# Performance work log

Hardware: AMD Instinct MI355X
Metric: run time of the kernel (lower is better)

## Reference

```python
import jax, jax.numpy as jnp
import numpy as np

S, B, E = 128, 64, 512          # seqlen, batch, incoming feature dim
P_LEN, P_DIM = 160, 512         # post length, post_size
H = 1024                        # hidden_size; GRU input_size = E + P_DIM = 1024
NEG = -1000000000.0             # masked_fill value in maskedSoftmax


def setup_inputs() -> dict:
    key = jax.random.key(0)
    ks = jax.random.split(key, 11)
    s = 1.0 / np.sqrt(H)
    u = lambda k, shp: jax.random.uniform(k, shp, jnp.float32, -s, s)
    return {
        "incoming": jax.random.normal(ks[0], (S, B, E), jnp.float32),
        "post": jax.random.normal(ks[1], (P_LEN, B, P_DIM), jnp.float32),
        "h_init": u(ks[2], (1, 1, H)),
        "weight_ih": u(ks[3], (3 * H, E + P_DIM)),
        "weight_hh": u(ks[4], (3 * H, H)),
        "bias_ih": u(ks[5], (3 * H,)),
        "bias_hh": u(ks[6], (3 * H,)),
        "wq": u(ks[7], (P_DIM, H)),
        "bq": u(ks[8], (P_DIM,)),
        "length": jax.random.randint(ks[9], (B,), 1, S + 1),
        "post_length": jax.random.randint(ks[10], (B,), 1, P_LEN + 1),
    }


def reference(incoming, post, h_init, weight_ih, weight_hh, bias_ih, bias_hh,
              wq, bq, length, post_length):
    seqlen, batch = incoming.shape[0], incoming.shape[1]
    plen = post.shape[0]
    h0 = jnp.broadcast_to(h_init[0], (batch, h_init.shape[-1]))  # h_init.repeat(1,B,1)[0]
    pos_mask = jnp.arange(plen)[:, None] < post_length[None, :]  # [P, B]

    def step(h, xt_i):
        xt, i = xt_i
        # attention over post, softmax along post-length axis (dim 0)
        query = h @ wq.T + bq                                   # [B, P_DIM]
        scores = jnp.einsum('pbd,bd->pb', post, query)          # [P, B]
        attn = jax.nn.softmax(jnp.where(pos_mask, scores, NEG), axis=0)
        context = jnp.einsum('pb,pbd->bd', attn, post)          # [B, P_DIM]
        x = jnp.concatenate([xt, context], axis=-1)             # [B, E + P_DIM]
        # torch GRUCell (gate order: r, z, n)
        gi = x @ weight_ih.T + bias_ih                          # [B, 3H]
        gh = h @ weight_hh.T + bias_hh                          # [B, 3H]
        i_r, i_z, i_n = jnp.split(gi, 3, axis=-1)
        h_r, h_z, h_n = jnp.split(gh, 3, axis=-1)
        r = jax.nn.sigmoid(i_r + h_r)
        z = jax.nn.sigmoid(i_z + h_z)
        n = jnp.tanh(i_n + r * h_n)
        h_new = (1.0 - z) * n + z * h
        # zero out finished sequences: h_now * (length > i)
        h_new = h_new * (length > i)[:, None].astype(h.dtype)
        return h_new, h_new

    h_last, hs = jax.lax.scan(step, h0, (incoming, jnp.arange(seqlen)))
    return hs, h_last
```

## Files before the change

### kernel.cpp

```cpp
#include <hip/hip_runtime.h>

#define S_LEN 128
#define BATCH 64
#define EDIM  512
#define PLEN  160
#define PDIM  512
#define HDIM  1024
#define G3    3072
#define NBLK  128
#define NTHR  256
#define PROWS 144

typedef _Float16 half8v  __attribute__((ext_vector_type(8)));
typedef _Float16 half4v  __attribute__((ext_vector_type(4)));
typedef _Float16 half2v  __attribute__((ext_vector_type(2)));
typedef float    f32x4   __attribute__((ext_vector_type(4)));

#define CTRL_UINTS 24576
#define OFF_CTRL ((size_t)0)
#define OFF_WIH  ((size_t)(CTRL_UINTS*4))
#define OFF_WHH  (OFF_WIH  + (size_t)G3*HDIM*2)
#define OFF_WQH  (OFF_WHH  + (size_t)G3*HDIM*2)
#define OFF_INC  (OFF_WQH  + (size_t)PDIM*HDIM*2)
#define OFF_POST (OFF_INC  + (size_t)S_LEN*BATCH*EDIM*2)
#define OFF_HH   (OFF_POST + (size_t)PLEN*BATCH*PDIM*2)
#define OFF_QH   (OFF_HH   + (size_t)BATCH*HDIM*2)
#define OFF_CTX  (OFF_QH   + (size_t)BATCH*PDIM*2)

__global__ void init_ctrl(unsigned* u) {
    int i = threadIdx.x + blockIdx.x * blockDim.x;
    if (i < CTRL_UINTS) u[i] = 0u;
}

__device__ __forceinline__ float wave_sum(float v) {
    v += __shfl_xor(v, 32); v += __shfl_xor(v, 16); v += __shfl_xor(v, 8);
    v += __shfl_xor(v, 4);  v += __shfl_xor(v, 2);  v += __shfl_xor(v, 1);
    return v;
}
__device__ __forceinline__ float wave_max(float v) {
    v = fmaxf(v, __shfl_xor(v, 32)); v = fmaxf(v, __shfl_xor(v, 16));
    v = fmaxf(v, __shfl_xor(v, 8));  v = fmaxf(v, __shfl_xor(v, 4));
    v = fmaxf(v, __shfl_xor(v, 2));  v = fmaxf(v, __shfl_xor(v, 1));
    return v;
}

__device__ __forceinline__ void gbar(unsigned* arrive, unsigned& gen, int tid, int blk) {
    gen++;
    __syncthreads();
    if (tid == 0)
        __hip_atomic_store(&arrive[blk * 32], gen, __ATOMIC_RELEASE, __HIP_MEMORY_SCOPE_AGENT);
    if (tid < NBLK) {
        unsigned* fl = &arrive[tid * 32];
        while (__hip_atomic_load(fl, __ATOMIC_RELAXED, __HIP_MEMORY_SCOPE_AGENT) < gen) { }
        __hip_atomic_load(fl, __ATOMIC_ACQUIRE, __HIP_MEMORY_SCOPE_AGENT);
    }
    __syncthreads();
}

__device__ __forceinline__ void mfma_acc(f32x4& acc, const _Float16* __restrict__ A, int lda,
                                         const _Float16* __restrict__ Bb, int ldb,
                                         int ksteps, int lane) {
    const _Float16* ap = A  + (size_t)(lane & 15) * lda + ((lane >> 4) << 3);
    const _Float16* bp = Bb + (size_t)(lane & 15) * ldb + ((lane >> 4) << 3);
    #pragma unroll
    for (int ks = 0; ks < ksteps; ++ks) {
        half8v av = *(const half8v*)ap;
        half8v bv = *(const half8v*)bp;
        acc = __builtin_amdgcn_mfma_f32_16x16x32_f16(av, bv, acc, 0, 0, 0);
        ap += 32; bp += 32;
    }
}

__device__ __forceinline__ void mfma_acc3(f32x4& a0, f32x4& a1, f32x4& a2,
        const _Float16* __restrict__ A, int lda,
        const _Float16* __restrict__ B0, const _Float16* __restrict__ B1,
        const _Float16* __restrict__ B2, int ldb, int ksteps, int lane) {
    const _Float16* ap = A  + (size_t)(lane & 15) * lda + ((lane >> 4) << 3);
    const _Float16* p0 = B0 + (size_t)(lane & 15) * ldb + ((lane >> 4) << 3);
    const _Float16* p1 = B1 + (size_t)(lane & 15) * ldb + ((lane >> 4) << 3);
    const _Float16* p2 = B2 + (size_t)(lane & 15) * ldb + ((lane >> 4) << 3);
    #pragma unroll
    for (int ks = 0; ks < ksteps; ++ks) {
        half8v av = *(const half8v*)ap;
        a0 = __builtin_amdgcn_mfma_f32_16x16x32_f16(av, *(const half8v*)p0, a0, 0, 0, 0);
        a1 = __builtin_amdgcn_mfma_f32_16x16x32_f16(av, *(const half8v*)p1, a1, 0, 0, 0);
        a2 = __builtin_amdgcn_mfma_f32_16x16x32_f16(av, *(const half8v*)p2, a2, 0, 0, 0);
        ap += 32; p0 += 32; p1 += 32; p2 += 32;
    }
}

__global__ __launch_bounds__(NTHR, 1) void gru_main(
    const float* __restrict__ incoming, const float* __restrict__ post,
    const float* __restrict__ h_init,   const float* __restrict__ w_ih,
    const float* __restrict__ w_hh,     const float* __restrict__ b_ih,
    const float* __restrict__ b_hh,     const float* __restrict__ wq,
    const float* __restrict__ bq,       const int* __restrict__ length,
    const int* __restrict__ post_length, float* __restrict__ out,
    char* __restrict__ ws)
{
    const int tid  = threadIdx.x;
    const int blk  = blockIdx.x;
    const int lane = tid & 63;
    const int wv   = tid >> 6;

    unsigned* arrive = (unsigned*)(ws + OFF_CTRL);
    unsigned* qflag  = (unsigned*)(ws + OFF_CTRL) + 4096;
    _Float16* wih_h  = (_Float16*)(ws + OFF_WIH);
    _Float16* whh_h  = (_Float16*)(ws + OFF_WHH);
    _Float16* wq_h   = (_Float16*)(ws + OFF_WQH);
    _Float16* inc_h  = (_Float16*)(ws + OFF_INC);
    _Float16* post_h = (_Float16*)(ws + OFF_POST);
    _Float16* h_h    = (_Float16*)(ws + OFF_HH);
    _Float16* query_h= (_Float16*)(ws + OFF_QH);
    _Float16* ctx_h  = (_Float16*)(ws + OFF_CTX);

    __shared__ __align__(16) _Float16 s_post[PROWS * PDIM];
    __shared__ __align__(16) _Float16 s_q[PDIM];
    __shared__ float s_scores[PLEN];
    __shared__ float s_w[PLEN];
    __shared__ float s_bc[2];

    unsigned gen = 0;

    float bsr = 0.f, bsz = 0.f, bin_ = 0.f, bhn = 0.f, bqv = 0.f;
    float hp[4] = {0.f, 0.f, 0.f, 0.f};
    int lenb[4] = {0, 0, 0, 0};
    int j0 = 0, ab = 0, plen = 0;
    if (blk < 64) {
        j0 = blk * 16;
        const int j = j0 + (lane & 15);
        bsr  = b_ih[j] + b_hh[j];
        bsz  = b_ih[HDIM + j] + b_hh[HDIM + j];
        bin_ = b_ih[2*HDIM + j];
        bhn  = b_hh[2*HDIM + j];
        if (blk < 32) bqv = bq[blk*16 + (lane & 15)];
        const float hi = h_init[j];
        const int r0 = wv*16 + ((lane >> 4) << 2);
        #pragma unroll
        for (int r = 0; r < 4; ++r) { hp[r] = hi; lenb[r] = length[r0 + r]; }
    } else {
        ab = blk - 64;
        plen = post_length[ab];
    }

    {
        const int NV4_W    = G3*HDIM/4;
        const int NV4_WQ   = PDIM*HDIM/4;
        const int NV4_INC  = S_LEN*BATCH*EDIM/4;
        const int NV4_POST = PLEN*BATCH*PDIM/4;
        const int TOT = 2*NV4_W + NV4_WQ + NV4_INC + NV4_POST;
        for (int i = blk*NTHR + tid; i < TOT; i += NBLK*NTHR) {
            const float* s; _Float16* dp; int o;
            if (i < NV4_W)                          { s = w_ih;     dp = wih_h;  o = i; }
            else if (i < 2*NV4_W)                   { s = w_hh;     dp = whh_h;  o = i - NV4_W; }
            else if (i < 2*NV4_W + NV4_WQ)          { s = wq;       dp = wq_h;   o = i - 2*NV4_W; }
            else if (i < 2*NV4_W + NV4_WQ + NV4_INC){ s = incoming; dp = inc_h;  o = i - 2*NV4_W - NV4_WQ; }
            else                                    { s = post;     dp = post_h; o = i - 2*NV4_W - NV4_WQ - NV4_INC; }
            f32x4 v = *(const f32x4*)(s + (size_t)o*4);
            half4v hv4 = {(_Float16)v.x, (_Float16)v.y, (_Float16)v.z, (_Float16)v.w};
            *(half4v*)(dp + (size_t)o*4) = hv4;
        }
        for (int i = blk*NTHR + tid; i < BATCH*HDIM; i += NBLK*NTHR)
            h_h[i] = (_Float16)h_init[i & (HDIM-1)];
    }
    if (blk >= 64) {
        for (int i = tid; i < PROWS*PDIM; i += NTHR) {
            const int p = i >> 9, d = i & (PDIM-1);
            s_post[i] = (_Float16)post[((size_t)p*BATCH + ab)*PDIM + d];
        }
    }
    gbar(arrive, gen, tid, blk);

    for (int t = 0; t < S_LEN; ++t) {
        f32x4 ghr = {0.f,0.f,0.f,0.f}, ghz = {0.f,0.f,0.f,0.f}, ghn_ = {0.f,0.f,0.f,0.f};
        f32x4 gir = {0.f,0.f,0.f,0.f}, giz = {0.f,0.f,0.f,0.f}, gin_ = {0.f,0.f,0.f,0.f};

        if (blk < 64) {
            if (blk < 32) {
                const int q0 = blk * 16;
                f32x4 qa = {0.f,0.f,0.f,0.f};
                mfma_acc(qa, h_h + (size_t)(wv*16)*HDIM, HDIM,
                         wq_h + (size_t)q0*HDIM, HDIM, HDIM/32, lane);
                const int q  = q0 + (lane & 15);
                const int r0 = wv*16 + ((lane >> 4) << 2);
                #pragma unroll
                for (int r = 0; r < 4; ++r)
                    query_h[(size_t)(r0+r)*PDIM + q] = (_Float16)(qa[r] + bqv);
                __syncthreads();
                if (tid == 0)
                    __hip_atomic_store(&qflag[blk * 32], (unsigned)(t+1),
                                       __ATOMIC_RELEASE, __HIP_MEMORY_SCOPE_AGENT);
            }
            mfma_acc3(ghr, ghz, ghn_, h_h + (size_t)(wv*16)*HDIM, HDIM,
                      whh_h + (size_t)j0*HDIM,
                      whh_h + (size_t)(HDIM + j0)*HDIM,
                      whh_h + (size_t)(2*HDIM + j0)*HDIM, HDIM, HDIM/32, lane);
            mfma_acc3(gir, giz, gin_, inc_h + ((size_t)t*BATCH + wv*16)*EDIM, EDIM,
                      wih_h + (size_t)j0*HDIM,
                      wih_h + (size_t)(HDIM + j0)*HDIM,
                      wih_h + (size_t)(2*HDIM + j0)*HDIM, HDIM, EDIM/32, lane);
        } else {
            half8v srow[4];
            #pragma unroll
            for (int i = 0; i < 4; ++i)
                srow[i] = *(const half8v*)(post_h +
                            ((size_t)(PROWS + wv + 4*i)*BATCH + ab)*PDIM + lane*8);
            if (tid < 32) {
                unsigned* fl = &qflag[tid * 32];
                while (__hip_atomic_load(fl, __ATOMIC_RELAXED, __HIP_MEMORY_SCOPE_AGENT) < (unsigned)(t+1)) { }
                __hip_atomic_load(fl, __ATOMIC_ACQUIRE, __HIP_MEMORY_SCOPE_AGENT);
            }
            __syncthreads();
            if (tid < PDIM/8)
                *(half8v*)&s_q[tid*8] = *(const half8v*)&query_h[(size_t)ab*PDIM + tid*8];
            __syncthreads();
            const half8v qv = *(const half8v*)&s_q[lane*8];
            #pragma unroll 2
            for (int p = wv; p < PROWS; p += 4) {
                const half8v pv = *(const half8v*)&s_post[(size_t)p*PDIM + lane*8];
                float sd = 0.f;
                #pragma unroll
                for (int jj = 0; jj < 8; ++jj) sd += (float)pv[jj] * (float)qv[jj];
                sd = wave_sum(sd);
                if (lane == 0) s_scores[p] = sd;
            }
            #pragma unroll
            for (int i = 0; i < 4; ++i) {
                const half8v pv = srow[i];
                float sd = 0.f;
                #pragma unroll
                for (int jj = 0; jj < 8; ++jj) sd += (float)pv[jj] * (float)qv[jj];
                sd = wave_sum(sd);
                if (lane == 0) s_scores[PROWS + wv + 4*i] = sd;
            }
            __syncthreads();
            if (wv == 0) {
                float m = -1e30f;
                for (int p = lane; p < plen; p += 64) m = fmaxf(m, s_scores[p]);
                m = wave_max(m);
                if (lane == 0) s_bc[0] = m;
            }
            __syncthreads();
            const float mx = s_bc[0];
            if (tid < PLEN) s_w[tid] = (tid < plen) ? __expf(s_scores[tid] - mx) : 0.f;
            __syncthreads();
            if (wv == 0) {
                float ss = 0.f;
                for (int p = lane; p < PLEN; p += 64) ss += s_w[p];
                ss = wave_sum(ss);
                if (lane == 0) s_bc[1] = 1.f / ss;
            }
            __syncthreads();
            const float inv_den = s_bc[1];
            const int d0 = tid << 1;
            float ca = 0.f, cb = 0.f;
            #pragma unroll 4
            for (int p = 0; p < PROWS; ++p) {
                const half2v pv2 = *(const half2v*)&s_post[(size_t)p*PDIM + d0];
                const float wp = s_w[p];
                ca += wp * (float)pv2[0];
                cb += wp * (float)pv2[1];
            }
            #pragma unroll 4
            for (int p = PROWS; p < PLEN; ++p) {
                const half2v pv2 = *(const half2v*)(post_h + ((size_t)p*BATCH + ab)*PDIM + d0);
                const float wp = s_w[p];
                ca += wp * (float)pv2[0];
                cb += wp * (float)pv2[1];
            }
            half2v cv; cv[0] = (_Float16)(ca * inv_den); cv[1] = (_Float16)(cb * inv_den);
            *(half2v*)&ctx_h[(size_t)ab*PDIM + d0] = cv;
        }
        gbar(arrive, gen, tid, blk);

        if (blk < 64) {
            mfma_acc3(gir, giz, gin_, ctx_h + (size_t)(wv*16)*PDIM, PDIM,
                      wih_h + (size_t)j0*HDIM + PDIM,
                      wih_h + (size_t)(HDIM + j0)*HDIM + PDIM,
                      wih_h + (size_t)(2*HDIM + j0)*HDIM + PDIM, HDIM, PDIM/32, lane);
            const int j  = j0 + (lane & 15);
            const int r0 = wv*16 + ((lane >> 4) << 2);
            #pragma unroll
            for (int r = 0; r < 4; ++r) {
                const int b = r0 + r;
                const float rg = 1.f / (1.f + __expf(-(gir[r] + ghr[r] + bsr)));
                const float zg = 1.f / (1.f + __expf(-(giz[r] + ghz[r] + bsz)));
                const float e2 = __expf(2.f * ((gin_[r] + bin_) + rg * (ghn_[r] + bhn)));
                const float ng = 1.f - 2.f / (e2 + 1.f);
                float hv = (1.f - zg) * ng + zg * hp[r];
                if (lenb[r] <= t) hv = 0.f;
                hp[r] = hv;
                out[(size_t)t*BATCH*HDIM + (size_t)b*HDIM + j] = hv;
                h_h[(size_t)b*HDIM + j] = (_Float16)hv;
                if (t == S_LEN - 1)
                    out[(size_t)S_LEN*BATCH*HDIM + (size_t)b*HDIM + j] = hv;
            }
        }
        if (t < S_LEN - 1) gbar(arrive, gen, tid, blk);
    }
}

extern "C" void kernel_launch(void* const* d_in, const int* in_sizes, int n_in,
                              void* d_out, int out_size, void* d_ws, size_t ws_size,
                              hipStream_t stream) {
    (void)in_sizes; (void)n_in; (void)out_size; (void)ws_size;
    const float* incoming    = (const float*)d_in[0];
    const float* post        = (const float*)d_in[1];
    const float* h_init      = (const float*)d_in[2];
    const float* w_ih        = (const float*)d_in[3];
    const float* w_hh        = (const float*)d_in[4];
    const float* b_ih        = (const float*)d_in[5];
    const float* b_hh        = (const float*)d_in[6];
    const float* wq          = (const float*)d_in[7];
    const float* bq          = (const float*)d_in[8];
    const int*   length      = (const int*)d_in[9];
    const int*   post_length = (const int*)d_in[10];
    float* out = (float*)d_out;

    init_ctrl<<<96, 256, 0, stream>>>((unsigned*)d_ws);
    gru_main<<<NBLK, NTHR, 0, stream>>>(incoming, post, h_init, w_ih, w_hh, b_ih, b_hh,
                                        wq, bq, length, post_length, out, (char*)d_ws);
}
```

Baseline: 5.778 ms.

## Replace persistent grid-barrier kernel with per-timestep kernel launches

The single persistent kernel, which used software grid barriers and flag spinning, is split into a staging kernel plus three kernels per timestep (query, attention, gate) launched 128 times. Kernel boundaries now provide the synchronisation, and a double-buffered fp16 hidden state replaces in-place updates. The cost is 384 extra launches, and the attention kernel reloads its post slice into shared memory on every step instead of keeping it resident. The query GEMM is also spread over 128 single-wave blocks instead of sharing blocks with the gate work.

```diff
diff --git a/kernel.cpp b/kernel.cpp
--- a/kernel.cpp
+++ b/kernel.cpp
@@ -7,8 +7,6 @@
 #define PDIM  512
 #define HDIM  1024
 #define G3    3072
-#define NBLK  128
-#define NTHR  256
 #define PROWS 144
 
 typedef _Float16 half8v  __attribute__((ext_vector_type(8)));
@@ -16,21 +14,14 @@
 typedef _Float16 half2v  __attribute__((ext_vector_type(2)));
 typedef float    f32x4   __attribute__((ext_vector_type(4)));
 
-#define CTRL_UINTS 24576
-#define OFF_CTRL ((size_t)0)
-#define OFF_WIH  ((size_t)(CTRL_UINTS*4))
+#define OFF_WIH  ((size_t)0)
 #define OFF_WHH  (OFF_WIH  + (size_t)G3*HDIM*2)
 #define OFF_WQH  (OFF_WHH  + (size_t)G3*HDIM*2)
 #define OFF_INC  (OFF_WQH  + (size_t)PDIM*HDIM*2)
 #define OFF_POST (OFF_INC  + (size_t)S_LEN*BATCH*EDIM*2)
-#define OFF_HH   (OFF_POST + (size_t)PLEN*BATCH*PDIM*2)
-#define OFF_QH   (OFF_HH   + (size_t)BATCH*HDIM*2)
+#define OFF_HB   (OFF_POST + (size_t)PLEN*BATCH*PDIM*2)
+#define OFF_QH   (OFF_HB   + (size_t)2*BATCH*HDIM*2)
 #define OFF_CTX  (OFF_QH   + (size_t)BATCH*PDIM*2)
-
-__global__ void init_ctrl(unsigned* u) {
-    int i = threadIdx.x + blockIdx.x * blockDim.x;
-    if (i < CTRL_UINTS) u[i] = 0u;
-}
 
 __device__ __forceinline__ float wave_sum(float v) {
     v += __shfl_xor(v, 32); v += __shfl_xor(v, 16); v += __shfl_xor(v, 8);
@@ -42,19 +33,6 @@
     v = fmaxf(v, __shfl_xor(v, 8));  v = fmaxf(v, __shfl_xor(v, 4));
     v = fmaxf(v, __shfl_xor(v, 2));  v = fmaxf(v, __shfl_xor(v, 1));
     return v;
-}
-
-__device__ __forceinline__ void gbar(unsigned* arrive, unsigned& gen, int tid, int blk) {
-    gen++;
-    __syncthreads();
-    if (tid == 0)
-        __hip_atomic_store(&arrive[blk * 32], gen, __ATOMIC_RELEASE, __HIP_MEMORY_SCOPE_AGENT);
-    if (tid < NBLK) {
-        unsigned* fl = &arrive[tid * 32];
-        while (__hip_atomic_load(fl, __ATOMIC_RELAXED, __HIP_MEMORY_SCOPE_AGENT) < gen) { }
-        __hip_atomic_load(fl, __ATOMIC_ACQUIRE, __HIP_MEMORY_SCOPE_AGENT);
-    }
-    __syncthreads();
 }
 
 __device__ __forceinline__ void mfma_acc(f32x4& acc, const _Float16* __restrict__ A, int lda,
@@ -89,30 +67,69 @@
     }
 }
 
-__global__ __launch_bounds__(NTHR, 1) void gru_main(
-    const float* __restrict__ incoming, const float* __restrict__ post,
-    const float* __restrict__ h_init,   const float* __restrict__ w_ih,
-    const float* __restrict__ w_hh,     const float* __restrict__ b_ih,
-    const float* __restrict__ b_hh,     const float* __restrict__ wq,
-    const float* __restrict__ bq,       const int* __restrict__ length,
-    const int* __restrict__ post_length, float* __restrict__ out,
+__global__ __launch_bounds__(256) void k_stage(
+    const float* __restrict__ w_ih, const float* __restrict__ w_hh,
+    const float* __restrict__ wq,   const float* __restrict__ incoming,
+    const float* __restrict__ post, const float* __restrict__ h_init,
     char* __restrict__ ws)
 {
-    const int tid  = threadIdx.x;
-    const int blk  = blockIdx.x;
-    const int lane = tid & 63;
-    const int wv   = tid >> 6;
-
-    unsigned* arrive = (unsigned*)(ws + OFF_CTRL);
-    unsigned* qflag  = (unsigned*)(ws + OFF_CTRL) + 4096;
     _Float16* wih_h  = (_Float16*)(ws + OFF_WIH);
     _Float16* whh_h  = (_Float16*)(ws + OFF_WHH);
     _Float16* wq_h   = (_Float16*)(ws + OFF_WQH);
     _Float16* inc_h  = (_Float16*)(ws + OFF_INC);
     _Float16* post_h = (_Float16*)(ws + OFF_POST);
-    _Float16* h_h    = (_Float16*)(ws + OFF_HH);
-    _Float16* query_h= (_Float16*)(ws + OFF_QH);
-    _Float16* ctx_h  = (_Float16*)(ws + OFF_CTX);
+    _Float16* hb     = (_Float16*)(ws + OFF_HB);
+    const int NV4_W    = G3*HDIM/4;
+    const int NV4_WQ   = PDIM*HDIM/4;
+    const int NV4_INC  = S_LEN*BATCH*EDIM/4;
+    const int NV4_POST = PLEN*BATCH*PDIM/4;
+    const int TOT = 2*NV4_W + NV4_WQ + NV4_INC + NV4_POST;
+    const int gs = gridDim.x * blockDim.x;
+    for (int i = blockIdx.x*blockDim.x + threadIdx.x; i < TOT; i += gs) {
+        const float* s; _Float16* dp; int o;
+        if (i < NV4_W)                          { s = w_ih;     dp = wih_h;  o = i; }
+        else if (i < 2*NV4_W)                   { s = w_hh;     dp = whh_h;  o = i - NV4_W; }
+        else if (i < 2*NV4_W + NV4_WQ)          { s = wq;       dp = wq_h;   o = i - 2*NV4_W; }
+        else if (i < 2*NV4_W + NV4_WQ + NV4_INC){ s = incoming; dp = inc_h;  o = i - 2*NV4_W - NV4_WQ; }
+        else                                    { s = post;     dp = post_h; o = i - 2*NV4_W - NV4_WQ - NV4_INC; }
+        f32x4 v = *(const f32x4*)(s + (size_t)o*4);
+        half4v hv4 = {(_Float16)v.x, (_Float16)v.y, (_Float16)v.z, (_Float16)v.w};
+        *(half4v*)(dp + (size_t)o*4) = hv4;
+    }
+    for (int i = blockIdx.x*blockDim.x + threadIdx.x; i < BATCH*HDIM; i += gs)
+        hb[i] = (_Float16)h_init[i & (HDIM-1)];
+}
+
+__global__ __launch_bounds__(64) void k_query(
+    const float* __restrict__ bq, int t, char* __restrict__ ws)
+{
+    const int lane = threadIdx.x;
+    const int mt = blockIdx.x >> 5;
+    const int nt = blockIdx.x & 31;
+    const _Float16* hb   = (const _Float16*)(ws + OFF_HB) + (size_t)(t & 1)*BATCH*HDIM;
+    const _Float16* wq_h = (const _Float16*)(ws + OFF_WQH);
+    _Float16* query_h    = (_Float16*)(ws + OFF_QH);
+    f32x4 qa = {0.f,0.f,0.f,0.f};
+    mfma_acc(qa, hb + (size_t)(mt*16)*HDIM, HDIM,
+             wq_h + (size_t)(nt*16)*HDIM, HDIM, HDIM/32, lane);
+    const int col = nt*16 + (lane & 15);
+    const int r0  = mt*16 + ((lane >> 4) << 2);
+    const float b = bq[col];
+    #pragma unroll
+    for (int r = 0; r < 4; ++r)
+        query_h[(size_t)(r0+r)*PDIM + col] = (_Float16)(qa[r] + b);
+}
+
+__global__ __launch_bounds__(256) void k_attn(
+    const int* __restrict__ post_length, int t, char* __restrict__ ws)
+{
+    const int tid  = threadIdx.x;
+    const int lane = tid & 63;
+    const int wv   = tid >> 6;
+    const int ab   = blockIdx.x;
+    const _Float16* post_h  = (const _Float16*)(ws + OFF_POST);
+    const _Float16* query_h = (const _Float16*)(ws + OFF_QH);
+    _Float16* ctx_h         = (_Float16*)(ws + OFF_CTX);
 
     __shared__ __align__(16) _Float16 s_post[PROWS * PDIM];
     __shared__ __align__(16) _Float16 s_q[PDIM];
@@ -120,183 +137,131 @@
     __shared__ float s_w[PLEN];
     __shared__ float s_bc[2];
 
-    unsigned gen = 0;
-
-    float bsr = 0.f, bsz = 0.f, bin_ = 0.f, bhn = 0.f, bqv = 0.f;
-    float hp[4] = {0.f, 0.f, 0.f, 0.f};
-    int lenb[4] = {0, 0, 0, 0};
-    int j0 = 0, ab = 0, plen = 0;
-    if (blk < 64) {
-        j0 = blk * 16;
-        const int j = j0 + (lane & 15);
-        bsr  = b_ih[j] + b_hh[j];
-        bsz  = b_ih[HDIM + j] + b_hh[HDIM + j];
-        bin_ = b_ih[2*HDIM + j];
-        bhn  = b_hh[2*HDIM + j];
-        if (blk < 32) bqv = bq[blk*16 + (lane & 15)];
-        const float hi = h_init[j];
-        const int r0 = wv*16 + ((lane >> 4) << 2);
+    const int plen = post_length[ab];
+    for (int i = tid; i < PROWS*PDIM/8; i += 256) {
+        const int p = i >> 6, v = i & 63;
+        ((half8v*)s_post)[i] = *(const half8v*)(post_h + ((size_t)p*BATCH + ab)*PDIM + v*8);
+    }
+    half8v srow[4];
+    #pragma unroll
+    for (int i = 0; i < 4; ++i)
+        srow[i] = *(const half8v*)(post_h + ((size_t)(PROWS + wv + 4*i)*BATCH + ab)*PDIM + lane*8);
+    if (tid < PDIM/8)
+        *(half8v*)&s_q[tid*8] = *(const half8v*)&query_h[(size_t)ab*PDIM + tid*8];
+    __syncthreads();
+
+    const half8v qv = *(const half8v*)&s_q[lane*8];
+    #pragma unroll 2
+    for (int p = wv; p < PROWS; p += 4) {
+        const half8v pv = *(const half8v*)&s_post[(size_t)p*PDIM + lane*8];
+        float sd = 0.f;
         #pragma unroll
-        for (int r = 0; r < 4; ++r) { hp[r] = hi; lenb[r] = length[r0 + r]; }
-    } else {
-        ab = blk - 64;
-        plen = post_length[ab];
-    }
-
-    {
-        const int NV4_W    = G3*HDIM/4;
-        const int NV4_WQ   = PDIM*HDIM/4;
-        const int NV4_INC  = S_LEN*BATCH*EDIM/4;
-        const int NV4_POST = PLEN*BATCH*PDIM/4;
-        const int TOT = 2*NV4_W + NV4_WQ + NV4_INC + NV4_POST;
-        for (int i = blk*NTHR + tid; i < TOT; i += NBLK*NTHR) {
-            const float* s; _Float16* dp; int o;
-            if (i < NV4_W)                          { s = w_ih;     dp = wih_h;  o = i; }
-            else if (i < 2*NV4_W)                   { s = w_hh;     dp = whh_h;  o = i - NV4_W; }
-            else if (i < 2*NV4_W + NV4_WQ)          { s = wq;       dp = wq_h;   o = i - 2*NV4_W; }
-            else if (i < 2*NV4_W + NV4_WQ + NV4_INC){ s = incoming; dp = inc_h;  o = i - 2*NV4_W - NV4_WQ; }
-            else                                    { s = post;     dp = post_h; o = i - 2*NV4_W - NV4_WQ - NV4_INC; }
-            f32x4 v = *(const f32x4*)(s + (size_t)o*4);
-            half4v hv4 = {(_Float16)v.x, (_Float16)v.y, (_Float16)v.z, (_Float16)v.w};
-            *(half4v*)(dp + (size_t)o*4) = hv4;
-        }
-        for (int i = blk*NTHR + tid; i < BATCH*HDIM; i += NBLK*NTHR)
-            h_h[i] = (_Float16)h_init[i & (HDIM-1)];
-    }
-    if (blk >= 64) {
-        for (int i = tid; i < PROWS*PDIM; i += NTHR) {
-            const int p = i >> 9, d = i & (PDIM-1);
-            s_post[i] = (_Float16)post[((size_t)p*BATCH + ab)*PDIM + d];
-        }
-    }
-    gbar(arrive, gen, tid, blk);
-
-    for (int t = 0; t < S_LEN; ++t) {
-        f32x4 ghr = {0.f,0.f,0.f,0.f}, ghz = {0.f,0.f,0.f,0.f}, ghn_ = {0.f,0.f,0.f,0.f};
-        f32x4 gir = {0.f,0.f,0.f,0.f}, giz = {0.f,0.f,0.f,0.f}, gin_ = {0.f,0.f,0.f,0.f};
-
-        if (blk < 64) {
-            if (blk < 32) {
-                const int q0 = blk * 16;
-                f32x4 qa = {0.f,0.f,0.f,0.f};
-                mfma_acc(qa, h_h + (size_t)(wv*16)*HDIM, HDIM,
-                         wq_h + (size_t)q0*HDIM, HDIM, HDIM/32, lane);
-                const int q  = q0 + (lane & 15);
-                const int r0 = wv*16 + ((lane >> 4) << 2);
-                #pragma unroll
-                for (int r = 0; r < 4; ++r)
-                    query_h[(size_t)(r0+r)*PDIM + q] = (_Float16)(qa[r] + bqv);
-                __syncthreads();
-                if (tid == 0)
-                    __hip_atomic_store(&qflag[blk * 32], (unsigned)(t+1),
-                                       __ATOMIC_RELEASE, __HIP_MEMORY_SCOPE_AGENT);
-            }
-            mfma_acc3(ghr, ghz, ghn_, h_h + (size_t)(wv*16)*HDIM, HDIM,
-                      whh_h + (size_t)j0*HDIM,
-                      whh_h + (size_t)(HDIM + j0)*HDIM,
-                      whh_h + (size_t)(2*HDIM + j0)*HDIM, HDIM, HDIM/32, lane);
-            mfma_acc3(gir, giz, gin_, inc_h + ((size_t)t*BATCH + wv*16)*EDIM, EDIM,
-                      wih_h + (size_t)j0*HDIM,
-                      wih_h + (size_t)(HDIM + j0)*HDIM,
-                      wih_h + (size_t)(2*HDIM + j0)*HDIM, HDIM, EDIM/32, lane);
-        } else {
-            half8v srow[4];
-            #pragma unroll
-            for (int i = 0; i < 4; ++i)
-                srow[i] = *(const half8v*)(post_h +
-                            ((size_t)(PROWS + wv + 4*i)*BATCH + ab)*PDIM + lane*8);
-            if (tid < 32) {
-                unsigned* fl = &qflag[tid * 32];
-                while (__hip_atomic_load(fl, __ATOMIC_RELAXED, __HIP_MEMORY_SCOPE_AGENT) < (unsigned)(t+1)) { }
-                __hip_atomic_load(fl, __ATOMIC_ACQUIRE, __HIP_MEMORY_SCOPE_AGENT);
-            }
-            __syncthreads();
-            if (tid < PDIM/8)
-                *(half8v*)&s_q[tid*8] = *(const half8v*)&query_h[(size_t)ab*PDIM + tid*8];
-            __syncthreads();
-            const half8v qv = *(const half8v*)&s_q[lane*8];
-            #pragma unroll 2
-            for (int p = wv; p < PROWS; p += 4) {
-                const half8v pv = *(const half8v*)&s_post[(size_t)p*PDIM + lane*8];
-                float sd = 0.f;
-                #pragma unroll
-                for (int jj = 0; jj < 8; ++jj) sd += (float)pv[jj] * (float)qv[jj];
-                sd = wave_sum(sd);
-                if (lane == 0) s_scores[p] = sd;
-            }
-            #pragma unroll
-            for (int i = 0; i < 4; ++i) {
-                const half8v pv = srow[i];
-                float sd = 0.f;
-                #pragma unroll
-                for (int jj = 0; jj < 8; ++jj) sd += (float)pv[jj] * (float)qv[jj];
-                sd = wave_sum(sd);
-                if (lane == 0) s_scores[PROWS + wv + 4*i] = sd;
-            }
-            __syncthreads();
-            if (wv == 0) {
-                float m = -1e30f;
-                for (int p = lane; p < plen; p += 64) m = fmaxf(m, s_scores[p]);
-                m = wave_max(m);
-                if (lane == 0) s_bc[0] = m;
-            }
-            __syncthreads();
-            const float mx = s_bc[0];
-            if (tid < PLEN) s_w[tid] = (tid < plen) ? __expf(s_scores[tid] - mx) : 0.f;
-            __syncthreads();
-            if (wv == 0) {
-                float ss = 0.f;
-                for (int p = lane; p < PLEN; p += 64) ss += s_w[p];
-                ss = wave_sum(ss);
-                if (lane == 0) s_bc[1] = 1.f / ss;
-            }
-            __syncthreads();
-            const float inv_den = s_bc[1];
-            const int d0 = tid << 1;
-            float ca = 0.f, cb = 0.f;
-            #pragma unroll 4
-            for (int p = 0; p < PROWS; ++p) {
-                const half2v pv2 = *(const half2v*)&s_post[(size_t)p*PDIM + d0];
-                const float wp = s_w[p];
-                ca += wp * (float)pv2[0];
-                cb += wp * (float)pv2[1];
-            }
-            #pragma unroll 4
-            for (int p = PROWS; p < PLEN; ++p) {
-                const half2v pv2 = *(const half2v*)(post_h + ((size_t)p*BATCH + ab)*PDIM + d0);
-                const float wp = s_w[p];
-                ca += wp * (float)pv2[0];
-                cb += wp * (float)pv2[1];
-            }
-            half2v cv; cv[0] = (_Float16)(ca * inv_den); cv[1] = (_Float16)(cb * inv_den);
-            *(half2v*)&ctx_h[(size_t)ab*PDIM + d0] = cv;
-        }
-        gbar(arrive, gen, tid, blk);
-
-        if (blk < 64) {
-            mfma_acc3(gir, giz, gin_, ctx_h + (size_t)(wv*16)*PDIM, PDIM,
-                      wih_h + (size_t)j0*HDIM + PDIM,
-                      wih_h + (size_t)(HDIM + j0)*HDIM + PDIM,
-                      wih_h + (size_t)(2*HDIM + j0)*HDIM + PDIM, HDIM, PDIM/32, lane);
-            const int j  = j0 + (lane & 15);
-            const int r0 = wv*16 + ((lane >> 4) << 2);
-            #pragma unroll
-            for (int r = 0; r < 4; ++r) {
-                const int b = r0 + r;
-                const float rg = 1.f / (1.f + __expf(-(gir[r] + ghr[r] + bsr)));
-                const float zg = 1.f / (1.f + __expf(-(giz[r] + ghz[r] + bsz)));
-                const float e2 = __expf(2.f * ((gin_[r] + bin_) + rg * (ghn_[r] + bhn)));
-                const float ng = 1.f - 2.f / (e2 + 1.f);
-                float hv = (1.f - zg) * ng + zg * hp[r];
-                if (lenb[r] <= t) hv = 0.f;
-                hp[r] = hv;
-                out[(size_t)t*BATCH*HDIM + (size_t)b*HDIM + j] = hv;
-                h_h[(size_t)b*HDIM + j] = (_Float16)hv;
-                if (t == S_LEN - 1)
-                    out[(size_t)S_LEN*BATCH*HDIM + (size_t)b*HDIM + j] = hv;
-            }
-        }
-        if (t < S_LEN - 1) gbar(arrive, gen, tid, blk);
+        for (int jj = 0; jj < 8; ++jj) sd += (float)pv[jj] * (float)qv[jj];
+        sd = wave_sum(sd);
+        if (lane == 0) s_scores[p] = sd;
+    }
+    #pragma unroll
+    for (int i = 0; i < 4; ++i) {
+        const half8v pv = srow[i];
+        float sd = 0.f;
+        #pragma unroll
+        for (int jj = 0; jj < 8; ++jj) sd += (float)pv[jj] * (float)qv[jj];
+        sd = wave_sum(sd);
+        if (lane == 0) s_scores[PROWS + wv + 4*i] = sd;
+    }
+    __syncthreads();
+    if (wv == 0) {
+        float m = -1e30f;
+        for (int p = lane; p < plen; p += 64) m = fmaxf(m, s_scores[p]);
+        m = wave_max(m);
+        if (lane == 0) s_bc[0] = m;
+    }
+    __syncthreads();
+    const float mx = s_bc[0];
+    if (tid < PLEN) s_w[tid] = (tid < plen) ? __expf(s_scores[tid] - mx) : 0.f;
+    __syncthreads();
+    if (wv == 0) {
+        float ss = 0.f;
+        for (int p = lane; p < PLEN; p += 64) ss += s_w[p];
+        ss = wave_sum(ss);
+        if (lane == 0) s_bc[1] = 1.f / ss;
+    }
+    __syncthreads();
+    const float inv_den = s_bc[1];
+    const int d0 = tid << 1;
+    float ca = 0.f, cb = 0.f;
+    #pragma unroll 4
+    for (int p = 0; p < PROWS; ++p) {
+        const half2v pv2 = *(const half2v*)&s_post[(size_t)p*PDIM + d0];
+        const float wp = s_w[p];
+        ca += wp * (float)pv2[0];
+        cb += wp * (float)pv2[1];
+    }
+    #pragma unroll 4
+    for (int p = PROWS; p < PLEN; ++p) {
+        const half2v pv2 = *(const half2v*)(post_h + ((size_t)p*BATCH + ab)*PDIM + d0);
+        const float wp = s_w[p];
+        ca += wp * (float)pv2[0];
+        cb += wp * (float)pv2[1];
+    }
+    half2v cv; cv[0] = (_Float16)(ca * inv_den); cv[1] = (_Float16)(cb * inv_den);
+    *(half2v*)&ctx_h[(size_t)ab*PDIM + d0] = cv;
+}
+
+__global__ __launch_bounds__(256) void k_gate(
+    const float* __restrict__ b_ih, const float* __restrict__ b_hh,
+    const float* __restrict__ h_init, const int* __restrict__ length,
+    float* __restrict__ out, int t, char* __restrict__ ws)
+{
+    const int tid  = threadIdx.x;
+    const int lane = tid & 63;
+    const int wv   = tid >> 6;
+    const int j0   = blockIdx.x * 16;
+    const _Float16* wih_h = (const _Float16*)(ws + OFF_WIH);
+    const _Float16* whh_h = (const _Float16*)(ws + OFF_WHH);
+    const _Float16* inc_h = (const _Float16*)(ws + OFF_INC);
+    const _Float16* ctx_h = (const _Float16*)(ws + OFF_CTX);
+    _Float16* hb          = (_Float16*)(ws + OFF_HB);
+    const _Float16* hin   = hb + (size_t)(t & 1)*BATCH*HDIM;
+    _Float16* hout        = hb + (size_t)((t + 1) & 1)*BATCH*HDIM;
+
+    const int j = j0 + (lane & 15);
+    const float bsr  = b_ih[j] + b_hh[j];
+    const float bsz  = b_ih[HDIM + j] + b_hh[HDIM + j];
+    const float bin_ = b_ih[2*HDIM + j];
+    const float bhn  = b_hh[2*HDIM + j];
+
+    f32x4 ghr = {0.f,0.f,0.f,0.f}, ghz = {0.f,0.f,0.f,0.f}, ghn_ = {0.f,0.f,0.f,0.f};
+    f32x4 gir = {0.f,0.f,0.f,0.f}, giz = {0.f,0.f,0.f,0.f}, gin_ = {0.f,0.f,0.f,0.f};
+    mfma_acc3(ghr, ghz, ghn_, hin + (size_t)(wv*16)*HDIM, HDIM,
+              whh_h + (size_t)j0*HDIM,
+              whh_h + (size_t)(HDIM + j0)*HDIM,
+              whh_h + (size_t)(2*HDIM + j0)*HDIM, HDIM, HDIM/32, lane);
+    mfma_acc3(gir, giz, gin_, inc_h + ((size_t)t*BATCH + wv*16)*EDIM, EDIM,
+              wih_h + (size_t)j0*HDIM,
+              wih_h + (size_t)(HDIM + j0)*HDIM,
+              wih_h + (size_t)(2*HDIM + j0)*HDIM, HDIM, EDIM/32, lane);
+    mfma_acc3(gir, giz, gin_, ctx_h + (size_t)(wv*16)*PDIM, PDIM,
+              wih_h + (size_t)j0*HDIM + PDIM,
+              wih_h + (size_t)(HDIM + j0)*HDIM + PDIM,
+              wih_h + (size_t)(2*HDIM + j0)*HDIM + PDIM, HDIM, PDIM/32, lane);
+
+    const int r0 = wv*16 + ((lane >> 4) << 2);
+    #pragma unroll
+    for (int r = 0; r < 4; ++r) {
+        const int b = r0 + r;
+        const float hp = (t == 0) ? h_init[j] : out[(size_t)(t-1)*BATCH*HDIM + (size_t)b*HDIM + j];
+        const int lenb = length[b];
+        const float rg = 1.f / (1.f + __expf(-(gir[r] + ghr[r] + bsr)));
+        const float zg = 1.f / (1.f + __expf(-(giz[r] + ghz[r] + bsz)));
+        const float e2 = __expf(2.f * ((gin_[r] + bin_) + rg * (ghn_[r] + bhn)));
+        const float ng = 1.f - 2.f / (e2 + 1.f);
+        float hv = (1.f - zg) * ng + zg * hp;
+        if (lenb <= t) hv = 0.f;
+        out[(size_t)t*BATCH*HDIM + (size_t)b*HDIM + j] = hv;
+        hout[(size_t)b*HDIM + j] = (_Float16)hv;
+        if (t == S_LEN - 1)
+            out[(size_t)S_LEN*BATCH*HDIM + (size_t)b*HDIM + j] = hv;
     }
 }
 
@@ -316,8 +281,12 @@
     const int*   length      = (const int*)d_in[9];
     const int*   post_length = (const int*)d_in[10];
     float* out = (float*)d_out;
-
-    init_ctrl<<<96, 256, 0, stream>>>((unsigned*)d_ws);
-    gru_main<<<NBLK, NTHR, 0, stream>>>(incoming, post, h_init, w_ih, w_hh, b_ih, b_hh,
-                                        wq, bq, length, post_length, out, (char*)d_ws);
-}
+    char* ws = (char*)d_ws;
+
+    k_stage<<<256, 256, 0, stream>>>(w_ih, w_hh, wq, incoming, post, h_init, ws);
+    for (int t = 0; t < S_LEN; ++t) {
+        k_query<<<128, 64, 0, stream>>>(bq, t, ws);
+        k_attn<<<64, 256, 0, stream>>>(post_length, t, ws);
+        k_gate<<<64, 256, 0, stream>>>(b_ih, b_hh, h_init, length, out, t, ws);
+    }
+}
```

New measurement: 7.299 ms. 1.26x slower.

## Compute query projection as split-K partials after each GRU update

Applied to the files above, without the earlier changes.

The separate per-step query GEMM (h @ wq^T on 32 blocks, followed by a flag wait) is removed. Each of the 64 GRU blocks now keeps its 16-column slice of wq in shared memory and, right after producing its h slice, writes a partial query product to global memory. The attention blocks then sum the 64 partials themselves, which takes the query computation and its flag synchronization off the critical path at the start of each step. The hidden state is double-buffered so the next step's read does not race with the current write. The cost is extra global traffic: 64×64×512 fp32 partial stores per step and a 64-way reduction in every attention block.

```diff
diff --git a/kernel.cpp b/kernel.cpp
--- a/kernel.cpp
+++ b/kernel.cpp
@@ -20,12 +20,11 @@
 #define OFF_CTRL ((size_t)0)
 #define OFF_WIH  ((size_t)(CTRL_UINTS*4))
 #define OFF_WHH  (OFF_WIH  + (size_t)G3*HDIM*2)
-#define OFF_WQH  (OFF_WHH  + (size_t)G3*HDIM*2)
-#define OFF_INC  (OFF_WQH  + (size_t)PDIM*HDIM*2)
+#define OFF_INC  (OFF_WHH  + (size_t)G3*HDIM*2)
 #define OFF_POST (OFF_INC  + (size_t)S_LEN*BATCH*EDIM*2)
-#define OFF_HH   (OFF_POST + (size_t)PLEN*BATCH*PDIM*2)
-#define OFF_QH   (OFF_HH   + (size_t)BATCH*HDIM*2)
-#define OFF_CTX  (OFF_QH   + (size_t)BATCH*PDIM*2)
+#define OFF_HB   (OFF_POST + (size_t)PLEN*BATCH*PDIM*2)
+#define OFF_CTX  (OFF_HB   + (size_t)2*BATCH*HDIM*2)
+#define OFF_QP   (OFF_CTX  + (size_t)BATCH*PDIM*2)
 
 __global__ void init_ctrl(unsigned* u) {
     int i = threadIdx.x + blockIdx.x * blockDim.x;
@@ -55,20 +54,6 @@
         __hip_atomic_load(fl, __ATOMIC_ACQUIRE, __HIP_MEMORY_SCOPE_AGENT);
     }
     __syncthreads();
-}
-
-__device__ __forceinline__ void mfma_acc(f32x4& acc, const _Float16* __restrict__ A, int lda,
-                                         const _Float16* __restrict__ Bb, int ldb,
-                                         int ksteps, int lane) {
-    const _Float16* ap = A  + (size_t)(lane & 15) * lda + ((lane >> 4) << 3);
-    const _Float16* bp = Bb + (size_t)(lane & 15) * ldb + ((lane >> 4) << 3);
-    #pragma unroll
-    for (int ks = 0; ks < ksteps; ++ks) {
-        half8v av = *(const half8v*)ap;
-        half8v bv = *(const half8v*)bp;
-        acc = __builtin_amdgcn_mfma_f32_16x16x32_f16(av, bv, acc, 0, 0, 0);
-        ap += 32; bp += 32;
-    }
 }
 
 __device__ __forceinline__ void mfma_acc3(f32x4& a0, f32x4& a1, f32x4& a2,
@@ -89,6 +74,24 @@
     }
 }
 
+__device__ __forceinline__ void qpart_mfma(const _Float16* s_hq, const _Float16* s_wqp,
+                                           float* __restrict__ qpart, int blk,
+                                           int lane, int wv) {
+    const int ko = (lane >> 4) << 3;
+    const half8v af = *(const half8v*)(s_hq + (size_t)(wv*16 + (lane & 15))*32 + ko);
+    const int b0 = wv*16 + ((lane >> 4) << 2);
+    #pragma unroll 4
+    for (int nt = 0; nt < 32; ++nt) {
+        const half8v bf = *(const half8v*)(s_wqp + (size_t)(nt*16 + (lane & 15))*32 + ko);
+        f32x4 acc = {0.f,0.f,0.f,0.f};
+        acc = __builtin_amdgcn_mfma_f32_16x16x32_f16(af, bf, acc, 0, 0, 0);
+        const int qc = nt*16 + (lane & 15);
+        #pragma unroll
+        for (int r = 0; r < 4; ++r)
+            qpart[((size_t)blk*BATCH + b0 + r)*PDIM + qc] = acc[r];
+    }
+}
+
 __global__ __launch_bounds__(NTHR, 1) void gru_main(
     const float* __restrict__ incoming, const float* __restrict__ post,
     const float* __restrict__ h_init,   const float* __restrict__ w_ih,
@@ -104,25 +107,25 @@
     const int wv   = tid >> 6;
 
     unsigned* arrive = (unsigned*)(ws + OFF_CTRL);
-    unsigned* qflag  = (unsigned*)(ws + OFF_CTRL) + 4096;
     _Float16* wih_h  = (_Float16*)(ws + OFF_WIH);
     _Float16* whh_h  = (_Float16*)(ws + OFF_WHH);
-    _Float16* wq_h   = (_Float16*)(ws + OFF_WQH);
     _Float16* inc_h  = (_Float16*)(ws + OFF_INC);
     _Float16* post_h = (_Float16*)(ws + OFF_POST);
-    _Float16* h_h    = (_Float16*)(ws + OFF_HH);
-    _Float16* query_h= (_Float16*)(ws + OFF_QH);
+    _Float16* hb     = (_Float16*)(ws + OFF_HB);
     _Float16* ctx_h  = (_Float16*)(ws + OFF_CTX);
+    float*    qpart  = (float*)(ws + OFF_QP);
 
     __shared__ __align__(16) _Float16 s_post[PROWS * PDIM];
     __shared__ __align__(16) _Float16 s_q[PDIM];
     __shared__ float s_scores[PLEN];
     __shared__ float s_w[PLEN];
     __shared__ float s_bc[2];
+    _Float16* s_wqp = s_post;
+    _Float16* s_hq  = s_post + 512*32;
 
     unsigned gen = 0;
 
-    float bsr = 0.f, bsz = 0.f, bin_ = 0.f, bhn = 0.f, bqv = 0.f;
+    float bsr = 0.f, bsz = 0.f, bin_ = 0.f, bhn = 0.f;
     float hp[4] = {0.f, 0.f, 0.f, 0.f};
     int lenb[4] = {0, 0, 0, 0};
     int j0 = 0, ab = 0, plen = 0;
@@ -133,7 +136,6 @@
         bsz  = b_ih[HDIM + j] + b_hh[HDIM + j];
         bin_ = b_ih[2*HDIM + j];
         bhn  = b_hh[2*HDIM + j];
-        if (blk < 32) bqv = bq[blk*16 + (lane & 15)];
         const float hi = h_init[j];
         const int r0 = wv*16 + ((lane >> 4) << 2);
         #pragma unroll
@@ -145,25 +147,34 @@
 
     {
         const int NV4_W    = G3*HDIM/4;
-        const int NV4_WQ   = PDIM*HDIM/4;
         const int NV4_INC  = S_LEN*BATCH*EDIM/4;
         const int NV4_POST = PLEN*BATCH*PDIM/4;
-        const int TOT = 2*NV4_W + NV4_WQ + NV4_INC + NV4_POST;
+        const int TOT = 2*NV4_W + NV4_INC + NV4_POST;
         for (int i = blk*NTHR + tid; i < TOT; i += NBLK*NTHR) {
             const float* s; _Float16* dp; int o;
-            if (i < NV4_W)                          { s = w_ih;     dp = wih_h;  o = i; }
-            else if (i < 2*NV4_W)                   { s = w_hh;     dp = whh_h;  o = i - NV4_W; }
-            else if (i < 2*NV4_W + NV4_WQ)          { s = wq;       dp = wq_h;   o = i - 2*NV4_W; }
-            else if (i < 2*NV4_W + NV4_WQ + NV4_INC){ s = incoming; dp = inc_h;  o = i - 2*NV4_W - NV4_WQ; }
-            else                                    { s = post;     dp = post_h; o = i - 2*NV4_W - NV4_WQ - NV4_INC; }
+            if (i < NV4_W)                  { s = w_ih;     dp = wih_h;  o = i; }
+            else if (i < 2*NV4_W)           { s = w_hh;     dp = whh_h;  o = i - NV4_W; }
+            else if (i < 2*NV4_W + NV4_INC) { s = incoming; dp = inc_h;  o = i - 2*NV4_W; }
+            else                            { s = post;     dp = post_h; o = i - 2*NV4_W - NV4_INC; }
             f32x4 v = *(const f32x4*)(s + (size_t)o*4);
             half4v hv4 = {(_Float16)v.x, (_Float16)v.y, (_Float16)v.z, (_Float16)v.w};
             *(half4v*)(dp + (size_t)o*4) = hv4;
         }
         for (int i = blk*NTHR + tid; i < BATCH*HDIM; i += NBLK*NTHR)
-            h_h[i] = (_Float16)h_init[i & (HDIM-1)];
-    }
-    if (blk >= 64) {
+            hb[i] = (_Float16)h_init[i & (HDIM-1)];
+    }
+    if (blk < 64) {
+        for (int i = tid; i < 512*32; i += NTHR) {
+            const int c = i >> 5, k = i & 31;
+            s_wqp[i] = (k < 16) ? (_Float16)wq[(size_t)c*HDIM + j0 + k] : (_Float16)0.f;
+        }
+        for (int i = tid; i < 64*32; i += NTHR) {
+            const int k = i & 31;
+            s_hq[i] = (k < 16) ? (_Float16)h_init[j0 + k] : (_Float16)0.f;
+        }
+        __syncthreads();
+        qpart_mfma(s_hq, s_wqp, qpart, blk, lane, wv);
+    } else {
         for (int i = tid; i < PROWS*PDIM; i += NTHR) {
             const int p = i >> 9, d = i & (PDIM-1);
             s_post[i] = (_Float16)post[((size_t)p*BATCH + ab)*PDIM + d];
@@ -176,22 +187,7 @@
         f32x4 gir = {0.f,0.f,0.f,0.f}, giz = {0.f,0.f,0.f,0.f}, gin_ = {0.f,0.f,0.f,0.f};
 
         if (blk < 64) {
-            if (blk < 32) {
-                const int q0 = blk * 16;
-                f32x4 qa = {0.f,0.f,0.f,0.f};
-                mfma_acc(qa, h_h + (size_t)(wv*16)*HDIM, HDIM,
-                         wq_h + (size_t)q0*HDIM, HDIM, HDIM/32, lane);
-                const int q  = q0 + (lane & 15);
-                const int r0 = wv*16 + ((lane >> 4) << 2);
-                #pragma unroll
-                for (int r = 0; r < 4; ++r)
-                    query_h[(size_t)(r0+r)*PDIM + q] = (_Float16)(qa[r] + bqv);
-                __syncthreads();
-                if (tid == 0)
-                    __hip_atomic_store(&qflag[blk * 32], (unsigned)(t+1),
-                                       __ATOMIC_RELEASE, __HIP_MEMORY_SCOPE_AGENT);
-            }
-            mfma_acc3(ghr, ghz, ghn_, h_h + (size_t)(wv*16)*HDIM, HDIM,
+            mfma_acc3(ghr, ghz, ghn_, hb + (size_t)(t & 1)*BATCH*HDIM + (size_t)(wv*16)*HDIM, HDIM,
                       whh_h + (size_t)j0*HDIM,
                       whh_h + (size_t)(HDIM + j0)*HDIM,
                       whh_h + (size_t)(2*HDIM + j0)*HDIM, HDIM, HDIM/32, lane);
@@ -205,14 +201,17 @@
             for (int i = 0; i < 4; ++i)
                 srow[i] = *(const half8v*)(post_h +
                             ((size_t)(PROWS + wv + 4*i)*BATCH + ab)*PDIM + lane*8);
-            if (tid < 32) {
-                unsigned* fl = &qflag[tid * 32];
-                while (__hip_atomic_load(fl, __ATOMIC_RELAXED, __HIP_MEMORY_SCOPE_AGENT) < (unsigned)(t+1)) { }
-                __hip_atomic_load(fl, __ATOMIC_ACQUIRE, __HIP_MEMORY_SCOPE_AGENT);
-            }
-            __syncthreads();
-            if (tid < PDIM/8)
-                *(half8v*)&s_q[tid*8] = *(const half8v*)&query_h[(size_t)ab*PDIM + tid*8];
+            {
+                const int c0 = tid << 1;
+                float qx = 0.f, qy = 0.f;
+                #pragma unroll 8
+                for (int k = 0; k < 64; ++k) {
+                    const float2 v = *(const float2*)&qpart[((size_t)k*BATCH + ab)*PDIM + c0];
+                    qx += v.x; qy += v.y;
+                }
+                s_q[c0]     = (_Float16)(qx + bq[c0]);
+                s_q[c0 + 1] = (_Float16)(qy + bq[c0 + 1]);
+            }
             __syncthreads();
             const half8v qv = *(const half8v*)&s_q[lane*8];
             #pragma unroll 2
@@ -278,8 +277,10 @@
                       wih_h + (size_t)j0*HDIM + PDIM,
                       wih_h + (size_t)(HDIM + j0)*HDIM + PDIM,
                       wih_h + (size_t)(2*HDIM + j0)*HDIM + PDIM, HDIM, PDIM/32, lane);
+            _Float16* hout = hb + (size_t)((t + 1) & 1)*BATCH*HDIM;
             const int j  = j0 + (lane & 15);
             const int r0 = wv*16 + ((lane >> 4) << 2);
+            float hvv[4];
             #pragma unroll
             for (int r = 0; r < 4; ++r) {
                 const int b = r0 + r;
@@ -289,12 +290,18 @@
                 const float ng = 1.f - 2.f / (e2 + 1.f);
                 float hv = (1.f - zg) * ng + zg * hp[r];
                 if (lenb[r] <= t) hv = 0.f;
-                hp[r] = hv;
+                hp[r] = hv; hvv[r] = hv;
                 out[(size_t)t*BATCH*HDIM + (size_t)b*HDIM + j] = hv;
-                h_h[(size_t)b*HDIM + j] = (_Float16)hv;
+                hout[(size_t)b*HDIM + j] = (_Float16)hv;
                 if (t == S_LEN - 1)
                     out[(size_t)S_LEN*BATCH*HDIM + (size_t)b*HDIM + j] = hv;
             }
+            __syncthreads();
+            #pragma unroll
+            for (int r = 0; r < 4; ++r)
+                s_hq[(size_t)(r0 + r)*32 + (lane & 15)] = (_Float16)hvv[r];
+            __syncthreads();
+            qpart_mfma(s_hq, s_wqp, qpart, blk, lane, wv);
         }
         if (t < S_LEN - 1) gbar(arrive, gen, tid, blk);
     }
```

Result: faster. 5.565 ms (-3.7%).
